# Optimization experiments

Measured on AMD Instinct MI355X. Metric: run time of the kernel, lower is better.

The kernel has to match this reference:

```python
import jax, jax.numpy as jnp
import numpy as np
from jax import lax

B, T, C = 64, 1024, 256


def setup_inputs() -> dict:
    key = jax.random.key(0)
    k1, k2 = jax.random.split(key)
    sequences = jax.random.normal(k1, (B, T, C), dtype=jnp.float32)
    transitions = jax.random.normal(k2, (C, C), dtype=jnp.float32)
    return {"sequences": sequences, "transitions": transitions}


def _viterbi_decode(sequences, transitions):
    # sequences: [B, T, C] unary scores; transitions: [C_prev, C_cur]
    num_classes = sequences.shape[-1]
    emissions = jnp.swapaxes(sequences, 0, 1)  # [T, B, C]

    def fwd_step(alpha, emit):
        # alpha: [B, C_prev]; emit: [B, C_cur]
        m = alpha[:, :, None] + transitions[None, :, :]  # [B, C_prev, C_cur]
        bp = jnp.argmax(m, axis=1).astype(jnp.int32)     # [B, C_cur] backpointers
        new_alpha = jnp.max(m, axis=1) + emit            # [B, C_cur]
        return new_alpha, bp

    alpha, bps = lax.scan(fwd_step, emissions[0], emissions[1:])  # bps: [T-1, B, C]
    last_tag = jnp.argmax(alpha, axis=-1).astype(jnp.int32)       # [B]

    def back_step(tag, bp):
        # tag: [B] tag at t+1; bp: [B, C] backpointers computed at step t+1
        prev = jnp.take_along_axis(bp, tag[:, None], axis=1)[:, 0]
        return prev, prev

    _, tags = lax.scan(back_step, last_tag, bps, reverse=True)  # [T-1, B]
    full = jnp.concatenate([tags, last_tag[None, :]], axis=0)   # [T, B]
    return jnp.swapaxes(full, 0, 1)  # [B, T]


def reference(sequences, transitions):
    # Inference path of CRF.call: viterbi decode + one-hot over num_classes.
    tags = _viterbi_decode(sequences, transitions)
    return jax.nn.one_hot(tags, sequences.shape[-1], dtype=sequences.dtype)
```

## Files before the change

### kernel.cpp

```cpp
#include <hip/hip_runtime.h>

#define Bn 64
#define Tn 1024
#define Cn 256

typedef float nv4 __attribute__((ext_vector_type(4)));

__device__ __forceinline__ float4 nt_load4(const float* p) {
  nv4 r = __builtin_nontemporal_load((const nv4*)p);
  return make_float4(r.x, r.y, r.z, r.w);
}
__device__ __forceinline__ void nt_store4(float* p, float4 v) {
  nv4 r = {v.x, v.y, v.z, v.w};
  __builtin_nontemporal_store(r, (nv4*)p);
}

template<int CTRL>
__device__ __forceinline__ float dpp_mov_f(float x) {
  return __int_as_float(__builtin_amdgcn_update_dpp(0, __float_as_int(x), CTRL, 0xF, 0xF, true));
}
template<int CTRL>
__device__ __forceinline__ void max_stage(float& v) {
  const float pv = __int_as_float(__builtin_amdgcn_update_dpp(
      (int)0xFF800000, __float_as_int(v), CTRL, 0xF, 0xF, false));
  v = fmaxf(v, pv);
}

__device__ __forceinline__ int argmax64_fast(float v, int i) {
  float mv = v;
  max_stage<0x111>(mv);
  max_stage<0x112>(mv);
  max_stage<0x114>(mv);
  max_stage<0x118>(mv);
  max_stage<0x142>(mv);
  max_stage<0x143>(mv);
  const float smax = __int_as_float(__builtin_amdgcn_readlane(__float_as_int(mv), 63));
  const unsigned long long m = __ballot(v == smax);
  const int ln = __ffsll((unsigned long long)m) - 1;
  return __builtin_amdgcn_readlane(i, ln);
}

__device__ __forceinline__ int apad(int m) { return (m >> 2) * 20 + (m & 3) * 4; }

__global__ __launch_bounds__(1024, 4) void crf_fwd_kernel(
    float* __restrict__ seq, const float* __restrict__ trans,
    float* __restrict__ transT, int useT) {
  __shared__ float lds[64 * 65];
  const int bi = blockIdx.x;
  const int tid = threadIdx.x;

  if (bi < Bn) {
    float* sb = seq + (size_t)bi * (Tn * Cn);
    const int l = tid & 63;
    const int w = tid >> 6;
    const int c = l & 15;
    const int g = l >> 4;
    const int ccb = w * 16 + g * 4;
    const int cpb = c * 16;
    float4 tr4[16];
#pragma unroll
    for (int k = 0; k < 16; ++k)
      tr4[k] = *(const float4*)(trans + (size_t)(cpb + k) * Cn + ccb);

    float* ab0 = lds;
    float* ab1 = lds + 320;
    if (tid < 64) *(float4*)(ab0 + apad(tid)) = ((const float4*)sb)[tid];
    const bool leader = (c == 0);
    const int woff = apad(w * 4 + g);
    float4 e4, pna;
    if (leader) e4 = *(const float4*)(sb + Cn + ccb);
    __syncthreads();

    for (int t = 1; t < Tn; ++t) {
      float4 pf;
      if (leader) {
        if (t > 1) *(float4*)(sb + (size_t)(t - 1) * Cn + ccb) = pna;
        const int tn = (t + 1 < Tn) ? (t + 1) : (Tn - 1);
        pf = *(const float4*)(sb + (size_t)tn * Cn + ccb);
      }
      const float* av = (t & 1) ? ab0 : ab1;
      float* aw = (t & 1) ? ab1 : ab0;
      const float* avc = av + c * 20;
      float m0 = -__builtin_inff(), m1 = m0, m2 = m0, m3 = m0;
#pragma unroll
      for (int j = 0; j < 4; ++j) {
        const float4 a = *(const float4*)(avc + j * 4);
        float4 t0 = tr4[4 * j + 0];
        m0 = fmaxf(m0, a.x + t0.x); m1 = fmaxf(m1, a.x + t0.y);
        m2 = fmaxf(m2, a.x + t0.z); m3 = fmaxf(m3, a.x + t0.w);
        float4 t1 = tr4[4 * j + 1];
        m0 = fmaxf(m0, a.y + t1.x); m1 = fmaxf(m1, a.y + t1.y);
        m2 = fmaxf(m2, a.y + t1.z); m3 = fmaxf(m3, a.y + t1.w);
        float4 t2 = tr4[4 * j + 2];
        m0 = fmaxf(m0, a.z + t2.x); m1 = fmaxf(m1, a.z + t2.y);
        m2 = fmaxf(m2, a.z + t2.z); m3 = fmaxf(m3, a.z + t2.w);
        float4 t3 = tr4[4 * j + 3];
        m0 = fmaxf(m0, a.w + t3.x); m1 = fmaxf(m1, a.w + t3.y);
        m2 = fmaxf(m2, a.w + t3.z); m3 = fmaxf(m3, a.w + t3.w);
      }
      m0 = fmaxf(m0, dpp_mov_f<0x128>(m0)); m1 = fmaxf(m1, dpp_mov_f<0x128>(m1));
      m2 = fmaxf(m2, dpp_mov_f<0x128>(m2)); m3 = fmaxf(m3, dpp_mov_f<0x128>(m3));
      m0 = fmaxf(m0, dpp_mov_f<0x124>(m0)); m1 = fmaxf(m1, dpp_mov_f<0x124>(m1));
      m2 = fmaxf(m2, dpp_mov_f<0x124>(m2)); m3 = fmaxf(m3, dpp_mov_f<0x124>(m3));
      m0 = fmaxf(m0, dpp_mov_f<0x122>(m0)); m1 = fmaxf(m1, dpp_mov_f<0x122>(m1));
      m2 = fmaxf(m2, dpp_mov_f<0x122>(m2)); m3 = fmaxf(m3, dpp_mov_f<0x122>(m3));
      m0 = fmaxf(m0, dpp_mov_f<0x121>(m0)); m1 = fmaxf(m1, dpp_mov_f<0x121>(m1));
      m2 = fmaxf(m2, dpp_mov_f<0x121>(m2)); m3 = fmaxf(m3, dpp_mov_f<0x121>(m3));
      if (leader) {
        float4 na;
        na.x = m0 + e4.x; na.y = m1 + e4.y; na.z = m2 + e4.z; na.w = m3 + e4.w;
        *(float4*)(aw + woff) = na;
        pna = na;
        e4 = pf;
      }
      __syncthreads();
    }
    if (leader) *(float4*)(sb + (size_t)(Tn - 1) * Cn + ccb) = pna;
  } else if (useT) {
    const int idx = bi - Bn;
    const int ti = idx >> 2, tj = idx & 3;
    const int tx = tid & 63, ty = tid >> 6;
#pragma unroll
    for (int q = 0; q < 4; ++q) {
      const int row = q * 16 + ty;
      lds[tx * 65 + row] = trans[(size_t)(ti * 64 + row) * Cn + tj * 64 + tx];
    }
    __syncthreads();
#pragma unroll
    for (int q = 0; q < 4; ++q) {
      const int row = q * 16 + ty;
      transT[(size_t)(tj * 64 + row) * Cn + ti * 64 + tx] = lds[row * 65 + tx];
    }
  }
}

__device__ __forceinline__ float4 onehot4(int tg, int cp0) {
  float4 z;
  z.x = (tg == cp0 + 0) ? 1.0f : 0.0f; z.y = (tg == cp0 + 1) ? 1.0f : 0.0f;
  z.z = (tg == cp0 + 2) ? 1.0f : 0.0f; z.w = (tg == cp0 + 3) ? 1.0f : 0.0f;
  return z;
}

template<int K>
__device__ __forceinline__ int chain_chunk(
    const float* __restrict__ A, int* __restrict__ tags,
    const float* __restrict__ transT, int tag, int l) {
  const int cp0 = l * 4;
#pragma unroll
  for (int k = 0; k < K; ++k) {
    const float4 tv = *(const float4*)(transT + (size_t)tag * Cn + cp0);
    const float4 ac = *(const float4*)(A + k * Cn + cp0);
    float v = ac.x + tv.x; int i = cp0;
    float vv; bool cnd;
    vv = ac.y + tv.y; cnd = vv > v; v = cnd ? vv : v; i = cnd ? cp0 + 1 : i;
    vv = ac.z + tv.z; cnd = vv > v; v = cnd ? vv : v; i = cnd ? cp0 + 2 : i;
    vv = ac.w + tv.w; cnd = vv > v; v = cnd ? vv : v; i = cnd ? cp0 + 3 : i;
    tag = argmax64_fast(v, i);
    if (l == 0) tags[k] = tag;
  }
  return tag;
}

__global__ __launch_bounds__(256) void crf_bwd_kernel(
    const float* __restrict__ seq, const float* __restrict__ trans,
    const float* __restrict__ transT, float* __restrict__ out, int useT) {
  __shared__ float aL[2][16][Cn];
  __shared__ int tagL[2][16];
  const int b = blockIdx.x;
  const int tid = threadIdx.x;
  const int wv = tid >> 6;
  const int l = tid & 63;
  const int cp0 = l * 4;
  const float* sb = seq + (size_t)b * (Tn * Cn);
  float* ob = out + (size_t)b * (Tn * Cn);

  if (!useT) {
    if (wv == 0) {
      float4 a = *(const float4*)(sb + (size_t)(Tn - 1) * Cn + cp0);
      float v = a.x; int i = cp0; bool cnd;
      cnd = a.y > v; v = cnd ? a.y : v; i = cnd ? cp0 + 1 : i;
      cnd = a.z > v; v = cnd ? a.z : v; i = cnd ? cp0 + 2 : i;
      cnd = a.w > v; v = cnd ? a.w : v; i = cnd ? cp0 + 3 : i;
      int tag = argmax64_fast(v, i);
      *(float4*)(ob + (size_t)(Tn - 1) * Cn + cp0) = onehot4(tag, cp0);
      for (int t = Tn - 2; t >= 0; --t) {
        const float4 ac = *(const float4*)(sb + (size_t)t * Cn + cp0);
        float4 tv;
        tv.x = trans[(size_t)(cp0 + 0) * Cn + tag];
        tv.y = trans[(size_t)(cp0 + 1) * Cn + tag];
        tv.z = trans[(size_t)(cp0 + 2) * Cn + tag];
        tv.w = trans[(size_t)(cp0 + 3) * Cn + tag];
        float v2 = ac.x + tv.x; int i2 = cp0; float vv; bool c2;
        vv = ac.y + tv.y; c2 = vv > v2; v2 = c2 ? vv : v2; i2 = c2 ? cp0 + 1 : i2;
        vv = ac.z + tv.z; c2 = vv > v2; v2 = c2 ? vv : v2; i2 = c2 ? cp0 + 2 : i2;
        vv = ac.w + tv.w; c2 = vv > v2; v2 = c2 ? vv : v2; i2 = c2 ? cp0 + 3 : i2;
        tag = argmax64_fast(v2, i2);
        *(float4*)(ob + (size_t)t * Cn + cp0) = onehot4(tag, cp0);
      }
    }
    return;
  }

  int tag = 0;
  if (wv == 0) {
    float4 a = *(const float4*)(sb + (size_t)(Tn - 1) * Cn + cp0);
    float v = a.x; int i = cp0; bool cnd;
    cnd = a.y > v; v = cnd ? a.y : v; i = cnd ? cp0 + 1 : i;
    cnd = a.z > v; v = cnd ? a.z : v; i = cnd ? cp0 + 2 : i;
    cnd = a.w > v; v = cnd ? a.w : v; i = cnd ? cp0 + 3 : i;
    tag = argmax64_fast(v, i);
    *(float4*)(ob + (size_t)(Tn - 1) * Cn + cp0) = onehot4(tag, cp0);
  } else if (wv <= 2) {
    const int s0 = (wv == 1) ? 0 : 8, s1 = (wv == 1) ? 8 : 15;
    for (int s = s0; s < s1; ++s)
      *(float4*)(&aL[0][s][cp0]) = nt_load4(sb + (size_t)(1022 - s) * Cn + cp0);
  }
  __syncthreads();

  int p = 0, t0 = 1022, K = 15, pt0 = 0, pK = 0;
  for (int ch = 0; ch < 64; ++ch) {
    const int nt0 = t0 - K;
    if (wv == 0) {
      if (ch == 0) tag = chain_chunk<15>(&aL[p][0][0], tagL[p], transT, tag, l);
      else        tag = chain_chunk<16>(&aL[p][0][0], tagL[p], transT, tag, l);
    } else if (wv <= 2) {
      if (ch < 63) {
        const int s0 = (wv == 1) ? 0 : 8, s1 = (wv == 1) ? 8 : 16;
        for (int s = s0; s < s1; ++s)
          *(float4*)(&aL[1 - p][s][cp0]) = nt_load4(sb + (size_t)(nt0 - s) * Cn + cp0);
      }
    } else {
      if (ch > 0) {
        for (int k = 0; k < pK; ++k)
          nt_store4(ob + (size_t)(pt0 - k) * Cn + cp0, onehot4(tagL[1 - p][k], cp0));
      }
    }
    __syncthreads();
    pt0 = t0; pK = K; t0 = nt0; K = 16; p ^= 1;
  }
  if (wv == 3) {
    for (int k = 0; k < 16; ++k)
      nt_store4(ob + (size_t)(15 - k) * Cn + cp0, onehot4(tagL[1][k], cp0));
  }
}

extern "C" void kernel_launch(void* const* d_in, const int* in_sizes, int n_in,
                              void* d_out, int out_size, void* d_ws, size_t ws_size,
                              hipStream_t stream) {
  float* seq = (float*)d_in[0];
  const float* trans = (const float*)d_in[1];
  float* out = (float*)d_out;
  float* transT = (float*)d_ws;
  const int useT = (ws_size >= (size_t)Cn * Cn * sizeof(float)) ? 1 : 0;

  crf_fwd_kernel<<<dim3(Bn + 16), dim3(1024), 0, stream>>>(seq, trans, transT, useT);
  crf_bwd_kernel<<<dim3(Bn), dim3(256), 0, stream>>>(seq, trans, transT, out, useT);
}
```

Baseline: 1.266 ms.

## Cache half of transposed transitions in LDS for backtrace; split max chains

The backward kernel now copies the first 127 rows of the transposed transition matrix into shared memory and serves backtrace lookups for tags below 127 from LDS instead of global memory. This shortens the latency of the serial, dependent backtrace chain for about half of the tags. The forward kernel now issues its four LDS alpha loads up front and splits the max reduction into two independent accumulator chains to expose more instruction-level parallelism. The risks are roughly 127 KB of extra LDS per backward block, which may cut occupancy or approach the LDS limit, and a data-dependent branch in the inner loop.

```diff
diff --git a/kernel.cpp b/kernel.cpp
--- a/kernel.cpp
+++ b/kernel.cpp
@@ -3,9 +3,9 @@
 #define Bn 64
 #define Tn 1024
 #define Cn 256
+#define TCROWS 127
 
 typedef float nv4 __attribute__((ext_vector_type(4)));
-
 __device__ __forceinline__ float4 nt_load4(const float* p) {
   nv4 r = __builtin_nontemporal_load((const nv4*)p);
   return make_float4(r.x, r.y, r.z, r.w);
@@ -42,6 +42,22 @@
 
 __device__ __forceinline__ int apad(int m) { return (m >> 2) * 20 + (m & 3) * 4; }
 
+#define MAC4(a_, jj, M0, M1, M2, M3)                                          \
+  {                                                                           \
+    const float4 t0 = tr4[4 * (jj) + 0];                                      \
+    M0 = fmaxf(M0, (a_).x + t0.x); M1 = fmaxf(M1, (a_).x + t0.y);             \
+    M2 = fmaxf(M2, (a_).x + t0.z); M3 = fmaxf(M3, (a_).x + t0.w);             \
+    const float4 t1 = tr4[4 * (jj) + 1];                                      \
+    M0 = fmaxf(M0, (a_).y + t1.x); M1 = fmaxf(M1, (a_).y + t1.y);             \
+    M2 = fmaxf(M2, (a_).y + t1.z); M3 = fmaxf(M3, (a_).y + t1.w);             \
+    const float4 t2 = tr4[4 * (jj) + 2];                                      \
+    M0 = fmaxf(M0, (a_).z + t2.x); M1 = fmaxf(M1, (a_).z + t2.y);             \
+    M2 = fmaxf(M2, (a_).z + t2.z); M3 = fmaxf(M3, (a_).z + t2.w);             \
+    const float4 t3 = tr4[4 * (jj) + 3];                                      \
+    M0 = fmaxf(M0, (a_).w + t3.x); M1 = fmaxf(M1, (a_).w + t3.y);             \
+    M2 = fmaxf(M2, (a_).w + t3.z); M3 = fmaxf(M3, (a_).w + t3.w);             \
+  }
+
 __global__ __launch_bounds__(1024, 4) void crf_fwd_kernel(
     float* __restrict__ seq, const float* __restrict__ trans,
     float* __restrict__ transT, int useT) {
@@ -72,32 +88,28 @@
     __syncthreads();
 
     for (int t = 1; t < Tn; ++t) {
+      const float* av = (t & 1) ? ab0 : ab1;
+      float* aw = (t & 1) ? ab1 : ab0;
+      const float* avc = av + c * 20;
+      const float4 a0 = *(const float4*)(avc + 0);
+      const float4 a1 = *(const float4*)(avc + 4);
+      const float4 a2 = *(const float4*)(avc + 8);
+      const float4 a3 = *(const float4*)(avc + 12);
       float4 pf;
       if (leader) {
         if (t > 1) *(float4*)(sb + (size_t)(t - 1) * Cn + ccb) = pna;
         const int tn = (t + 1 < Tn) ? (t + 1) : (Tn - 1);
         pf = *(const float4*)(sb + (size_t)tn * Cn + ccb);
       }
-      const float* av = (t & 1) ? ab0 : ab1;
-      float* aw = (t & 1) ? ab1 : ab0;
-      const float* avc = av + c * 20;
-      float m0 = -__builtin_inff(), m1 = m0, m2 = m0, m3 = m0;
-#pragma unroll
-      for (int j = 0; j < 4; ++j) {
-        const float4 a = *(const float4*)(avc + j * 4);
-        float4 t0 = tr4[4 * j + 0];
-        m0 = fmaxf(m0, a.x + t0.x); m1 = fmaxf(m1, a.x + t0.y);
-        m2 = fmaxf(m2, a.x + t0.z); m3 = fmaxf(m3, a.x + t0.w);
-        float4 t1 = tr4[4 * j + 1];
-        m0 = fmaxf(m0, a.y + t1.x); m1 = fmaxf(m1, a.y + t1.y);
-        m2 = fmaxf(m2, a.y + t1.z); m3 = fmaxf(m3, a.y + t1.w);
-        float4 t2 = tr4[4 * j + 2];
-        m0 = fmaxf(m0, a.z + t2.x); m1 = fmaxf(m1, a.z + t2.y);
-        m2 = fmaxf(m2, a.z + t2.z); m3 = fmaxf(m3, a.z + t2.w);
-        float4 t3 = tr4[4 * j + 3];
-        m0 = fmaxf(m0, a.w + t3.x); m1 = fmaxf(m1, a.w + t3.y);
-        m2 = fmaxf(m2, a.w + t3.z); m3 = fmaxf(m3, a.w + t3.w);
-      }
+      const float ninf = -__builtin_inff();
+      float p0 = ninf, p1 = ninf, p2 = ninf, p3 = ninf;
+      float q0 = ninf, q1 = ninf, q2 = ninf, q3 = ninf;
+      MAC4(a0, 0, p0, p1, p2, p3)
+      MAC4(a2, 2, q0, q1, q2, q3)
+      MAC4(a1, 1, p0, p1, p2, p3)
+      MAC4(a3, 3, q0, q1, q2, q3)
+      float m0 = fmaxf(p0, q0), m1 = fmaxf(p1, q1);
+      float m2 = fmaxf(p2, q2), m3 = fmaxf(p3, q3);
       m0 = fmaxf(m0, dpp_mov_f<0x128>(m0)); m1 = fmaxf(m1, dpp_mov_f<0x128>(m1));
       m2 = fmaxf(m2, dpp_mov_f<0x128>(m2)); m3 = fmaxf(m3, dpp_mov_f<0x128>(m3));
       m0 = fmaxf(m0, dpp_mov_f<0x124>(m0)); m1 = fmaxf(m1, dpp_mov_f<0x124>(m1));
@@ -144,11 +156,17 @@
 template<int K>
 __device__ __forceinline__ int chain_chunk(
     const float* __restrict__ A, int* __restrict__ tags,
-    const float* __restrict__ transT, int tag, int l) {
+    const float* __restrict__ transT, const float* __restrict__ tc,
+    int tag, int l) {
   const int cp0 = l * 4;
 #pragma unroll
   for (int k = 0; k < K; ++k) {
-    const float4 tv = *(const float4*)(transT + (size_t)tag * Cn + cp0);
+    float4 tv;
+    if (tag < TCROWS) {
+      tv = *(const float4*)(tc + tag * Cn + cp0);
+    } else {
+      tv = *(const float4*)(transT + (size_t)tag * Cn + cp0);
+    }
     const float4 ac = *(const float4*)(A + k * Cn + cp0);
     float v = ac.x + tv.x; int i = cp0;
     float vv; bool cnd;
@@ -165,6 +183,7 @@
     const float* __restrict__ seq, const float* __restrict__ trans,
     const float* __restrict__ transT, float* __restrict__ out, int useT) {
   __shared__ float aL[2][16][Cn];
+  __shared__ float tc[TCROWS * Cn];
   __shared__ int tagL[2][16];
   const int b = blockIdx.x;
   const int tid = threadIdx.x;
@@ -201,6 +220,13 @@
     return;
   }
 
+  {
+    const int r0 = wv * 32;
+    const int r1 = (r0 + 32 < TCROWS) ? (r0 + 32) : TCROWS;
+    for (int r = r0; r < r1; ++r)
+      *(float4*)(&tc[r * Cn + cp0]) = *(const float4*)(transT + (size_t)r * Cn + cp0);
+  }
+
   int tag = 0;
   if (wv == 0) {
     float4 a = *(const float4*)(sb + (size_t)(Tn - 1) * Cn + cp0);
@@ -221,8 +247,8 @@
   for (int ch = 0; ch < 64; ++ch) {
     const int nt0 = t0 - K;
     if (wv == 0) {
-      if (ch == 0) tag = chain_chunk<15>(&aL[p][0][0], tagL[p], transT, tag, l);
-      else        tag = chain_chunk<16>(&aL[p][0][0], tagL[p], transT, tag, l);
+      if (ch == 0) tag = chain_chunk<15>(&aL[p][0][0], tagL[p], transT, tc, tag, l);
+      else        tag = chain_chunk<16>(&aL[p][0][0], tagL[p], transT, tc, tag, l);
     } else if (wv <= 2) {
       if (ch < 63) {
         const int s0 = (wv == 1) ? 0 : 8, s1 = (wv == 1) ? 8 : 16;
```

New measurement: 1.261 ms. About the same (-0.4%).
